# Kernel tuning notes

Hardware: AMD Instinct MI355X
Metric: run time of the kernel (lower is better)

Reference implementation:

```python
import jax, jax.numpy as jnp
import numpy as np

N_QUBITS = 8
N_Q_LAYERS = 4
TARGET = 0
B, N, H = 64, 512, 512


def _apply_1q(state, U, w):
    # apply 2x2 complex gate U on wire w of state with shape (2,)*n
    state = jnp.tensordot(U, state, axes=((1,), (w,)))
    return jnp.moveaxis(state, 0, w)


def _cnot(state, c, t):
    s0 = jnp.take(state, 0, axis=c)
    s1 = jnp.take(state, 1, axis=c)
    t_ = t - 1 if t > c else t
    s1 = jnp.flip(s1, axis=t_)  # X on target where control=1
    return jnp.stack([s0, s1], axis=c)


def _ry(theta):
    c, s = jnp.cos(theta / 2), jnp.sin(theta / 2)
    return jnp.stack([jnp.stack([c, -s]), jnp.stack([s, c])]).astype(jnp.complex64)


def _rx(theta):
    c, s = jnp.cos(theta / 2), jnp.sin(theta / 2)
    z = jnp.zeros_like(c)
    re = jnp.stack([jnp.stack([c, z]), jnp.stack([z, c])])
    im = jnp.stack([jnp.stack([z, s]), jnp.stack([s, z])])
    return (re.astype(jnp.complex64) - 1j * im.astype(jnp.complex64))


def _circuit(angles, weights):
    # AngleEmbedding(rotation='Y') + BasicEntanglerLayers(RX + CNOT ring) + <Z_i>
    n = N_QUBITS
    state = jnp.zeros((2,) * n, dtype=jnp.complex64).at[(0,) * n].set(1.0)
    for w in range(n):
        state = _apply_1q(state, _ry(angles[w]), w)
    for l in range(N_Q_LAYERS):
        for w in range(n):
            state = _apply_1q(state, _rx(weights[l, w]), w)
        for w in range(n):
            state = _cnot(state, w, (w + 1) % n)
    probs = state.real ** 2 + state.imag ** 2
    zs = []
    for i in range(n):
        p = probs.sum(axis=tuple(a for a in range(n) if a != i))  # [2]
        zs.append(p[0] - p[1])
    return jnp.stack(zs)  # [n_qubits]


def setup_inputs() -> dict:
    key = jax.random.key(0)
    ks = jax.random.split(key, 10)
    adj = jax.random.uniform(ks[1], (N, N), dtype=jnp.float32)
    norm_adj = adj / adj.sum(axis=1, keepdims=True)  # row-normalized adjacency
    sH = 1.0 / np.sqrt(H)
    return {
        "x": jax.random.normal(ks[0], (B, N, H), dtype=jnp.float32),
        "norm_adj": norm_adj,
        "W_gcn_w": jax.random.normal(ks[2], (H, H), dtype=jnp.float32) * sH,
        "W_gcn_b": jax.random.normal(ks[3], (H,), dtype=jnp.float32) * sH,
        "pre_w": jax.random.normal(ks[4], (N_QUBITS, H), dtype=jnp.float32) * sH,
        "pre_b": jax.random.normal(ks[5], (N_QUBITS,), dtype=jnp.float32) * sH,
        "post_w": jax.random.normal(ks[6], (H, N_QUBITS), dtype=jnp.float32) * (1.0 / np.sqrt(N_QUBITS)),
        "post_b": jax.random.normal(ks[7], (H,), dtype=jnp.float32) * (1.0 / np.sqrt(N_QUBITS)),
        "q_weights": jax.random.uniform(ks[8], (N_Q_LAYERS, N_QUBITS), dtype=jnp.float32) * 2.0 * jnp.pi,
    }


def reference(x, norm_adj, W_gcn_w, W_gcn_b, pre_w, pre_b, post_w, post_b, q_weights):
    # classical GCN aggregation over all N nodes
    x_agg = jnp.einsum('ij,bjh->bih', norm_adj, x)  # [B,N,H]
    x_agg = jax.nn.gelu(x_agg @ W_gcn_w.T + W_gcn_b, approximate=False)
    # dropout is identity in eval mode
    tgt = x_agg[:, TARGET, :]  # [B,H]
    x_qin = jnp.tanh(tgt @ pre_w.T + pre_b) * jnp.pi  # [B,n_qubits]
    q_out = jax.vmap(lambda a: _circuit(a, q_weights))(x_qin)  # [B,n_qubits]
    q_out = q_out @ post_w.T + post_b  # [B,H]
    out = x_agg.at[:, TARGET, :].set(q_out)
    return out
```

## Files before the change

kernel.cpp:

```cpp
#include <hip/hip_runtime.h>
#include <hip/hip_bf16.h>
#include <math.h>

#define B_  64
#define D_  512
#define NQ  8
#define NL  4

typedef __bf16 bf16;
typedef float  f32x4  __attribute__((ext_vector_type(4)));
typedef bf16   bf16x8 __attribute__((ext_vector_type(8)));

__device__ __forceinline__ void async_load16(const bf16* g, bf16* l) {
    __builtin_amdgcn_global_load_lds(
        (const __attribute__((address_space(1))) void*)g,
        (__attribute__((address_space(3))) void*)l, 16, 0, 0);
}

__global__ __launch_bounds__(256) void convert_kernel(const float* __restrict__ src,
                                                      bf16* __restrict__ dst, int n8) {
    int i = blockIdx.x * 256 + threadIdx.x;
    if (i < n8) {
        const float4 v0 = *(const float4*)(src + (size_t)i * 8);
        const float4 v1 = *(const float4*)(src + (size_t)i * 8 + 4);
        bf16x8 p;
        p[0] = (bf16)v0.x; p[1] = (bf16)v0.y; p[2] = (bf16)v0.z; p[3] = (bf16)v0.w;
        p[4] = (bf16)v1.x; p[5] = (bf16)v1.y; p[6] = (bf16)v1.z; p[7] = (bf16)v1.w;
        *(bf16x8*)(dst + (size_t)i * 8) = p;
    }
}

template <int GELU>
__global__ __launch_bounds__(256) void gemm_nt_pipe(const bf16* __restrict__ A,
                                                    const bf16* __restrict__ Bv,
                                                    const float* __restrict__ bias,
                                                    void* __restrict__ Cout) {
    __shared__ bf16 SA[2][128 * 64];
    __shared__ bf16 SB[2][128 * 64];
    const int b    = blockIdx.y;
    const int tile = blockIdx.x;
    const int m0   = (tile >> 2) * 128;
    const int n0   = (tile & 3) * 128;
    const int t    = threadIdx.x;
    const int lane = t & 63;
    const int w    = t >> 6;
    const int wr   = (w >> 1) * 64;
    const int wc   = (w & 1) * 64;
    const int l15  = lane & 15;
    const int quad = lane >> 4;

    f32x4 acc[4][4];
    for (int i = 0; i < 4; i++)
        for (int j = 0; j < 4; j++) acc[i][j] = (f32x4)(0.0f);

    const bf16* Bb = Bv + (size_t)b * D_ * D_;

    const int rl = lane >> 3;
    const int ck = (lane & 7) ^ rl;

    #define ISSUE_STEP(KK, BUF)                                                          \
        {                                                                                \
            const int k0_ = (KK) * 64;                                                   \
            _Pragma("unroll")                                                            \
            for (int j = 0; j < 4; j++) {                                                \
                int rbase = w * 32 + j * 8;                                              \
                async_load16(A  + (size_t)(m0 + rbase + rl) * D_ + k0_ + ck * 8,         \
                             &SA[BUF][rbase * 64]);                                      \
                async_load16(Bb + (size_t)(n0 + rbase + rl) * D_ + k0_ + ck * 8,         \
                             &SB[BUF][rbase * 64]);                                      \
            }                                                                            \
        }

    ISSUE_STEP(0, 0);

    #pragma unroll
    for (int k = 0; k < 8; k++) {
        const int cur = k & 1;
        if (k < 7) {
            ISSUE_STEP(k + 1, (k + 1) & 1);
            asm volatile("s_waitcnt vmcnt(8)" ::: "memory");
        } else {
            asm volatile("s_waitcnt vmcnt(0)" ::: "memory");
        }
        __builtin_amdgcn_s_barrier();

        #pragma unroll
        for (int kk = 0; kk < 2; kk++) {
            bf16x8 af[4], bfr[4];
            #pragma unroll
            for (int mt = 0; mt < 4; mt++) {
                int row = wr + mt * 16 + l15;
                int s   = (kk * 4 + quad) ^ (l15 & 7);
                af[mt] = *(const bf16x8*)&SA[cur][row * 64 + s * 8];
            }
            #pragma unroll
            for (int nt = 0; nt < 4; nt++) {
                int row = wc + nt * 16 + l15;
                int s   = (kk * 4 + quad) ^ (l15 & 7);
                bfr[nt] = *(const bf16x8*)&SB[cur][row * 64 + s * 8];
            }
            #pragma unroll
            for (int mt = 0; mt < 4; mt++)
                #pragma unroll
                for (int nt = 0; nt < 4; nt++)
                    acc[mt][nt] = __builtin_amdgcn_mfma_f32_16x16x32_bf16(af[mt], bfr[nt], acc[mt][nt], 0, 0, 0);
        }
        __builtin_amdgcn_s_barrier();
    }
    #undef ISSUE_STEP

    if (GELU == 0) {
        bf16* Cb = (bf16*)Cout + (size_t)b * D_ * D_;
        for (int mt = 0; mt < 4; mt++) {
            int row = m0 + wr + mt * 16 + quad * 4;
            for (int nt = 0; nt < 4; nt++) {
                int col = n0 + wc + nt * 16 + l15;
                for (int r = 0; r < 4; r++)
                    Cb[(size_t)(row + r) * D_ + col] = (bf16)acc[mt][nt][r];
            }
        }
    } else {
        float* Cb = (float*)Cout + (size_t)b * D_ * D_;
        for (int mt = 0; mt < 4; mt++) {
            int row = m0 + wr + mt * 16 + quad * 4;
            for (int nt = 0; nt < 4; nt++) {
                int col = n0 + wc + nt * 16 + l15;
                float bv = bias[col];
                for (int r = 0; r < 4; r++) {
                    float v = acc[mt][nt][r] + bv;
                    Cb[(size_t)(row + r) * D_ + col] = 0.5f * v * (1.0f + erff(v * 0.70710678118654752f));
                }
            }
        }
    }
}

__global__ __launch_bounds__(64) void quantum_kernel(float* __restrict__ out,
                                                     const float* __restrict__ pre_w,
                                                     const float* __restrict__ pre_b,
                                                     const float* __restrict__ post_w,
                                                     const float* __restrict__ post_b,
                                                     const float* __restrict__ qw) {
    const int b = blockIdx.x;
    const int l = threadIdx.x;
    float* row0 = out + (size_t)b * D_ * D_;

    float tg[8];
    #pragma unroll
    for (int j = 0; j < 8; j++) tg[j] = row0[l + 64 * j];

    float ang[NQ];
    #pragma unroll
    for (int q = 0; q < NQ; q++) {
        float s = 0.f;
        #pragma unroll
        for (int j = 0; j < 8; j++) s += tg[j] * pre_w[q * D_ + l + 64 * j];
        #pragma unroll
        for (int m = 32; m >= 1; m >>= 1) s += __shfl_xor(s, m, 64);
        ang[q] = tanhf(s + pre_b[q]) * 3.14159265358979323846f;
    }

    float cw[NQ], sw[NQ];
    #pragma unroll
    for (int w = 0; w < NQ; w++) { cw[w] = cosf(0.5f * ang[w]); sw[w] = sinf(0.5f * ang[w]); }
    float re[4], im[4];
    #pragma unroll
    for (int r = 0; r < 4; r++) {
        int idx = l * 4 + r;
        float a = 1.f;
        #pragma unroll
        for (int w = 0; w < NQ; w++) a *= ((idx >> (7 - w)) & 1) ? sw[w] : cw[w];
        re[r] = a; im[r] = 0.f;
    }

    for (int lay = 0; lay < NL; lay++) {
        #pragma unroll
        for (int w = 0; w < 6; w++) {
            float th = 0.5f * qw[lay * NQ + w];
            float c = cosf(th), s = sinf(th);
            int m = 1 << (5 - w);
            #pragma unroll
            for (int r = 0; r < 4; r++) {
                float pre_ = __shfl_xor(re[r], m, 64);
                float pim_ = __shfl_xor(im[r], m, 64);
                re[r] = c * re[r] + s * pim_;
                im[r] = c * im[r] - s * pre_;
            }
        }
        {
            float th = 0.5f * qw[lay * NQ + 6];
            float c = cosf(th), s = sinf(th);
            float or0 = re[0], or1 = re[1], or2 = re[2], or3 = re[3];
            float oi0 = im[0], oi1 = im[1], oi2 = im[2], oi3 = im[3];
            re[0] = c * or0 + s * oi2;  im[0] = c * oi0 - s * or2;
            re[1] = c * or1 + s * oi3;  im[1] = c * oi1 - s * or3;
            re[2] = c * or2 + s * oi0;  im[2] = c * oi2 - s * or0;
            re[3] = c * or3 + s * oi1;  im[3] = c * oi3 - s * or1;
        }
        {
            float th = 0.5f * qw[lay * NQ + 7];
            float c = cosf(th), s = sinf(th);
            float or0 = re[0], or1 = re[1], or2 = re[2], or3 = re[3];
            float oi0 = im[0], oi1 = im[1], oi2 = im[2], oi3 = im[3];
            re[0] = c * or0 + s * oi1;  im[0] = c * oi0 - s * or1;
            re[1] = c * or1 + s * oi0;  im[1] = c * oi1 - s * or0;
            re[2] = c * or2 + s * oi3;  im[2] = c * oi2 - s * or3;
            re[3] = c * or3 + s * oi2;  im[3] = c * oi3 - s * or2;
        }
        #pragma unroll
        for (int w = 0; w < 5; w++) {
            int cb = 7 - w, tb = 6 - w;
            int tm = 1 << (tb - 2);
            bool ctl = (l >> (cb - 2)) & 1;
            #pragma unroll
            for (int r = 0; r < 4; r++) {
                float pre_ = __shfl_xor(re[r], tm, 64);
                float pim_ = __shfl_xor(im[r], tm, 64);
                re[r] = ctl ? pre_ : re[r];
                im[r] = ctl ? pim_ : im[r];
            }
        }
        {
            bool ctl = l & 1;
            float t0 = re[0], t1 = re[1], t2 = re[2], t3 = re[3];
            float u0 = im[0], u1 = im[1], u2 = im[2], u3 = im[3];
            re[0] = ctl ? t2 : t0;  re[1] = ctl ? t3 : t1;
            re[2] = ctl ? t0 : t2;  re[3] = ctl ? t1 : t3;
            im[0] = ctl ? u2 : u0;  im[1] = ctl ? u3 : u1;
            im[2] = ctl ? u0 : u2;  im[3] = ctl ? u1 : u3;
        }
        {
            float t2 = re[2], t3 = re[3], u2 = im[2], u3 = im[3];
            re[2] = t3; re[3] = t2; im[2] = u3; im[3] = u2;
        }
        {
            #pragma unroll
            for (int r = 0; r < 4; r++) {
                float pre_ = __shfl_xor(re[r], 32, 64);
                float pim_ = __shfl_xor(im[r], 32, 64);
                if (r & 1) { re[r] = pre_; im[r] = pim_; }
            }
        }
    }

    float pr[4];
    #pragma unroll
    for (int r = 0; r < 4; r++) pr[r] = re[r] * re[r] + im[r] * im[r];
    float z[NQ];
    #pragma unroll
    for (int q = 0; q < NQ; q++) {
        int bit = 7 - q;
        float s = 0.f;
        #pragma unroll
        for (int r = 0; r < 4; r++) {
            int idx = l * 4 + r;
            s += ((idx >> bit) & 1) ? -pr[r] : pr[r];
        }
        #pragma unroll
        for (int m = 32; m >= 1; m >>= 1) s += __shfl_xor(s, m, 64);
        z[q] = s;
    }

    #pragma unroll
    for (int j = 0; j < 8; j++) {
        int h = l + 64 * j;
        float v = post_b[h];
        #pragma unroll
        for (int q = 0; q < NQ; q++) v += z[q] * post_w[h * NQ + q];
        row0[h] = v;
    }
}

extern "C" void kernel_launch(void* const* d_in, const int* in_sizes, int n_in,
                              void* d_out, int out_size, void* d_ws, size_t ws_size,
                              hipStream_t stream) {
    const float* x        = (const float*)d_in[0];
    const float* norm_adj = (const float*)d_in[1];
    const float* W_gcn_w  = (const float*)d_in[2];
    const float* W_gcn_b  = (const float*)d_in[3];
    const float* pre_w    = (const float*)d_in[4];
    const float* pre_b    = (const float*)d_in[5];
    const float* post_w   = (const float*)d_in[6];
    const float* post_b   = (const float*)d_in[7];
    const float* q_w      = (const float*)d_in[8];
    float* out = (float*)d_out;

    bf16* xbf = (bf16*)d_out;
    bf16* Yt  = (bf16*)d_ws;
    const size_t MB32 = (size_t)32 * 1024 * 1024;
    bf16* Wbf   = (bf16*)((char*)d_ws + MB32);
    bf16* adjbf = Wbf + D_ * D_;

    const int n8_x = B_ * D_ * D_ / 8;
    const int n8_m = D_ * D_ / 8;
    convert_kernel<<<(n8_m + 255) / 256, 256, 0, stream>>>(W_gcn_w, Wbf, n8_m);
    convert_kernel<<<(n8_m + 255) / 256, 256, 0, stream>>>(norm_adj, adjbf, n8_m);
    convert_kernel<<<(n8_x + 255) / 256, 256, 0, stream>>>(x, xbf, n8_x);

    dim3 grid(16, B_);
    gemm_nt_pipe<0><<<grid, 256, 0, stream>>>(Wbf, xbf, nullptr, (void*)Yt);
    gemm_nt_pipe<1><<<grid, 256, 0, stream>>>(adjbf, Yt, W_gcn_b, (void*)out);

    quantum_kernel<<<B_, 64, 0, stream>>>(out, pre_w, pre_b, post_w, post_b, q_w);
}
```

Measured before the change: 204.5 us.

## Halve GEMM K-tile to 32 with new swizzle and merge conversion launches

```diff
diff --git a/kernel.cpp b/kernel.cpp
--- a/kernel.cpp
+++ b/kernel.cpp
@@ -17,17 +17,21 @@
         (__attribute__((address_space(3))) void*)l, 16, 0, 0);
 }
 
-__global__ __launch_bounds__(256) void convert_kernel(const float* __restrict__ src,
-                                                      bf16* __restrict__ dst, int n8) {
+__global__ __launch_bounds__(256) void convert3_kernel(const float* __restrict__ s0, bf16* __restrict__ d0, int n0,
+                                                       const float* __restrict__ s1, bf16* __restrict__ d1, int n1,
+                                                       const float* __restrict__ s2, bf16* __restrict__ d2, int n2) {
     int i = blockIdx.x * 256 + threadIdx.x;
-    if (i < n8) {
-        const float4 v0 = *(const float4*)(src + (size_t)i * 8);
-        const float4 v1 = *(const float4*)(src + (size_t)i * 8 + 4);
-        bf16x8 p;
-        p[0] = (bf16)v0.x; p[1] = (bf16)v0.y; p[2] = (bf16)v0.z; p[3] = (bf16)v0.w;
-        p[4] = (bf16)v1.x; p[5] = (bf16)v1.y; p[6] = (bf16)v1.z; p[7] = (bf16)v1.w;
-        *(bf16x8*)(dst + (size_t)i * 8) = p;
-    }
+    const float* s; bf16* d;
+    if (i < n0)                { s = s0; d = d0; }
+    else if (i < n0 + n1)      { s = s1; d = d1; i -= n0; }
+    else if (i < n0 + n1 + n2) { s = s2; d = d2; i -= n0 + n1; }
+    else return;
+    const float4 v0 = *(const float4*)(s + (size_t)i * 8);
+    const float4 v1 = *(const float4*)(s + (size_t)i * 8 + 4);
+    bf16x8 p;
+    p[0] = (bf16)v0.x; p[1] = (bf16)v0.y; p[2] = (bf16)v0.z; p[3] = (bf16)v0.w;
+    p[4] = (bf16)v1.x; p[5] = (bf16)v1.y; p[6] = (bf16)v1.z; p[7] = (bf16)v1.w;
+    *(bf16x8*)(d + (size_t)i * 8) = p;
 }
 
 template <int GELU>
@@ -35,8 +39,8 @@
                                                     const bf16* __restrict__ Bv,
                                                     const float* __restrict__ bias,
                                                     void* __restrict__ Cout) {
-    __shared__ bf16 SA[2][128 * 64];
-    __shared__ bf16 SB[2][128 * 64];
+    __shared__ bf16 SA[2][128 * 32];
+    __shared__ bf16 SB[2][128 * 32];
     const int b    = blockIdx.y;
     const int tile = blockIdx.x;
     const int m0   = (tile >> 2) * 128;
@@ -55,56 +59,54 @@
 
     const bf16* Bb = Bv + (size_t)b * D_ * D_;
 
-    const int rl = lane >> 3;
-    const int ck = (lane & 7) ^ rl;
+    const int rl = lane >> 2;
+    const int ck = (lane & 3) ^ ((lane >> 4) & 3);
 
     #define ISSUE_STEP(KK, BUF)                                                          \
         {                                                                                \
-            const int k0_ = (KK) * 64;                                                   \
+            const int k0_ = (KK) * 32;                                                   \
             _Pragma("unroll")                                                            \
-            for (int j = 0; j < 4; j++) {                                                \
-                int rbase = w * 32 + j * 8;                                              \
+            for (int j = 0; j < 2; j++) {                                                \
+                int rbase = w * 32 + j * 16;                                             \
                 async_load16(A  + (size_t)(m0 + rbase + rl) * D_ + k0_ + ck * 8,         \
-                             &SA[BUF][rbase * 64]);                                      \
+                             &SA[BUF][rbase * 32]);                                      \
                 async_load16(Bb + (size_t)(n0 + rbase + rl) * D_ + k0_ + ck * 8,         \
-                             &SB[BUF][rbase * 64]);                                      \
+                             &SB[BUF][rbase * 32]);                                      \
             }                                                                            \
         }
 
     ISSUE_STEP(0, 0);
 
     #pragma unroll
-    for (int k = 0; k < 8; k++) {
+    for (int k = 0; k < 16; k++) {
         const int cur = k & 1;
-        if (k < 7) {
+        if (k < 15) {
             ISSUE_STEP(k + 1, (k + 1) & 1);
-            asm volatile("s_waitcnt vmcnt(8)" ::: "memory");
+            asm volatile("s_waitcnt vmcnt(4)" ::: "memory");
         } else {
             asm volatile("s_waitcnt vmcnt(0)" ::: "memory");
         }
         __builtin_amdgcn_s_barrier();
 
-        #pragma unroll
-        for (int kk = 0; kk < 2; kk++) {
-            bf16x8 af[4], bfr[4];
+        bf16x8 af[4], bfr[4];
+        #pragma unroll
+        for (int mt = 0; mt < 4; mt++) {
+            int row = wr + mt * 16 + l15;
+            int s   = quad ^ (l15 >> 2);
+            af[mt] = *(const bf16x8*)&SA[cur][row * 32 + s * 8];
+        }
+        #pragma unroll
+        for (int nt = 0; nt < 4; nt++) {
+            int row = wc + nt * 16 + l15;
+            int s   = quad ^ (l15 >> 2);
+            bfr[nt] = *(const bf16x8*)&SB[cur][row * 32 + s * 8];
+        }
+        #pragma unroll
+        for (int mt = 0; mt < 4; mt++)
             #pragma unroll
-            for (int mt = 0; mt < 4; mt++) {
-                int row = wr + mt * 16 + l15;
-                int s   = (kk * 4 + quad) ^ (l15 & 7);
-                af[mt] = *(const bf16x8*)&SA[cur][row * 64 + s * 8];
-            }
-            #pragma unroll
-            for (int nt = 0; nt < 4; nt++) {
-                int row = wc + nt * 16 + l15;
-                int s   = (kk * 4 + quad) ^ (l15 & 7);
-                bfr[nt] = *(const bf16x8*)&SB[cur][row * 64 + s * 8];
-            }
-            #pragma unroll
-            for (int mt = 0; mt < 4; mt++)
-                #pragma unroll
-                for (int nt = 0; nt < 4; nt++)
-                    acc[mt][nt] = __builtin_amdgcn_mfma_f32_16x16x32_bf16(af[mt], bfr[nt], acc[mt][nt], 0, 0, 0);
-        }
+            for (int nt = 0; nt < 4; nt++)
+                acc[mt][nt] = __builtin_amdgcn_mfma_f32_16x16x32_bf16(af[mt], bfr[nt], acc[mt][nt], 0, 0, 0);
+
         __builtin_amdgcn_s_barrier();
     }
     #undef ISSUE_STEP
@@ -293,9 +295,8 @@
 
     const int n8_x = B_ * D_ * D_ / 8;
     const int n8_m = D_ * D_ / 8;
-    convert_kernel<<<(n8_m + 255) / 256, 256, 0, stream>>>(W_gcn_w, Wbf, n8_m);
-    convert_kernel<<<(n8_m + 255) / 256, 256, 0, stream>>>(norm_adj, adjbf, n8_m);
-    convert_kernel<<<(n8_x + 255) / 256, 256, 0, stream>>>(x, xbf, n8_x);
+    convert3_kernel<<<(n8_x + 2 * n8_m + 255) / 256, 256, 0, stream>>>(
+        x, xbf, n8_x, W_gcn_w, Wbf, n8_m, norm_adj, adjbf, n8_m);
 
     dim3 grid(16, B_);
     gemm_nt_pipe<0><<<grid, 256, 0, stream>>>(Wbf, xbf, nullptr, (void*)Yt);
```

New measurement: 209.2 us. 2.3% more time.
